# Kernel tuning notes

Hardware: AMD Instinct MI355X
Metric: run time of the kernel (lower is better)

Reference implementation:

```python
import jax, jax.numpy as jnp
import numpy as np

HIDDEN = 4096
N_HEADS = 32
N_KV_HEADS = 8
HEAD_DIM = 128
ROPE_BASE = 10000.0


def setup_inputs() -> dict:
    key = jax.random.key(0)
    k1, k2, k3, k4, k5 = jax.random.split(key, 5)
    s = 0.02  # init scale for weights
    return {
        "hidden_states": jax.random.normal(k1, (1, 2048, HIDDEN), dtype=jnp.float32),
        "Wq": jax.random.normal(k2, (N_HEADS * HEAD_DIM, HIDDEN), dtype=jnp.float32) * s,
        "Wk": jax.random.normal(k3, (N_KV_HEADS * HEAD_DIM, HIDDEN), dtype=jnp.float32) * s,
        "Wv": jax.random.normal(k4, (N_KV_HEADS * HEAD_DIM, HIDDEN), dtype=jnp.float32) * s,
        "Wo": jax.random.normal(k5, (HIDDEN, HIDDEN), dtype=jnp.float32) * s,
    }


def _rope(x, cos, sin):
    # x: [B, H, T, D]; cos/sin: [T, D/2] -> rotate split halves (Llama style)
    d2 = x.shape[-1] // 2
    x1, x2 = x[..., :d2], x[..., d2:]
    return jnp.concatenate([x1 * cos - x2 * sin, x1 * sin + x2 * cos], axis=-1)


def reference(hidden_states, Wq, Wk, Wv, Wo):
    B, T, _ = hidden_states.shape
    H, Hkv, D = N_HEADS, N_KV_HEADS, HEAD_DIM
    G = H // Hkv  # kv groups

    q = jnp.einsum("bth,qh->btq", hidden_states, Wq).reshape(B, T, H, D).transpose(0, 2, 1, 3)
    k = jnp.einsum("bth,kh->btk", hidden_states, Wk).reshape(B, T, Hkv, D).transpose(0, 2, 1, 3)
    v = jnp.einsum("bth,vh->btv", hidden_states, Wv).reshape(B, T, Hkv, D).transpose(0, 2, 1, 3)

    # RoPE (position_offset = 0)
    positions = jnp.arange(T, dtype=jnp.float32)
    inv_freq = ROPE_BASE ** (-jnp.arange(0, D, 2, dtype=jnp.float32) / D)  # [D/2]
    angles = positions[:, None] * inv_freq[None, :]                        # [T, D/2]
    cos, sin = jnp.cos(angles), jnp.sin(angles)
    q = _rope(q, cos, sin)
    k = _rope(k, cos, sin)

    # GQA attention without materializing expanded K/V: group query heads
    qg = q.reshape(B, Hkv, G, T, D)
    scale = 1.0 / jnp.sqrt(jnp.asarray(D, dtype=q.dtype))
    scores = jnp.einsum("bkgtd,bksd->bkgts", qg, k) * scale  # [B, Hkv, G, T, T]
    causal = jnp.tril(jnp.ones((T, T), dtype=bool))
    scores = jnp.where(causal, scores, jnp.finfo(scores.dtype).min)
    probs = jax.nn.softmax(scores, axis=-1)
    attn = jnp.einsum("bkgts,bksd->bkgtd", probs, v)          # [B, Hkv, G, T, D]
    attn = attn.reshape(B, H, T, D).transpose(0, 2, 1, 3).reshape(B, T, H * D)

    return jnp.einsum("btq,oq->bto", attn, Wo)
```

## Files before the change

### kernel.cpp

```cpp
#include <hip/hip_runtime.h>
#include <stdint.h>

#define T_SEQ   2048
#define HID     4096
#define NH      32
#define NKV     8
#define HD      128
#define QCOLS   6144
#define QK_SCALE 0.08838834764831845f

typedef _Float16 half_t;
typedef _Float16 half8 __attribute__((ext_vector_type(8)));
typedef _Float16 half4v __attribute__((ext_vector_type(4)));
typedef float    f32x4 __attribute__((ext_vector_type(4)));

typedef __attribute__((address_space(1))) const void cg_void;
typedef __attribute__((address_space(3))) void lds_void;

__global__ __launch_bounds__(256) void cast_all_k(const float* __restrict__ X,
                                                  const float* __restrict__ Wq,
                                                  const float* __restrict__ Wk,
                                                  const float* __restrict__ Wv,
                                                  const float* __restrict__ Wo,
                                                  half_t* __restrict__ Xh,
                                                  half_t* __restrict__ Wqkvh,
                                                  half_t* __restrict__ Woh) {
  int i = blockIdx.x * 256 + threadIdx.x;
  const float* src; half_t* dst; int off;
  if (i < 2097152)      { src = X;  dst = Xh;               off = i; }
  else if (i < 6291456) { src = Wq; dst = Wqkvh;            off = i - 2097152; }
  else if (i < 7340032) { src = Wk; dst = Wqkvh + 16777216; off = i - 6291456; }
  else if (i < 8388608) { src = Wv; dst = Wqkvh + 20971520; off = i - 7340032; }
  else                  { src = Wo; dst = Woh;              off = i - 8388608; }
  f32x4 v = *(const f32x4*)(src + (size_t)off * 4);
  half4v o;
  o[0] = (half_t)v[0]; o[1] = (half_t)v[1]; o[2] = (half_t)v[2]; o[3] = (half_t)v[3];
  *(half4v*)(dst + (size_t)off * 4) = o;
}

__global__ __launch_bounds__(256) void rope_tables_k(float* __restrict__ cs) {
  int idx = blockIdx.x * 256 + threadIdx.x;
  int t = idx >> 6, i = idx & 63;
  float inv = expf(-(float)i * 0.14391156831212787f);
  float a = (float)t * inv;
  cs[idx] = cosf(a);
  cs[131072 + idx] = sinf(a);
}

__global__ __launch_bounds__(256) void rope_vt_k(half_t* __restrict__ QKV,
                                                 const float* __restrict__ cs,
                                                 half_t* __restrict__ Vt) {
  if (blockIdx.x < 20480) {
    int idx = blockIdx.x * 256 + threadIdx.x;
    int i = idx & 63;
    int rem = idx >> 6;
    int head = rem % 40;
    int t = rem / 40;
    int colbase = (head < 32) ? head * HD : HID + (head - 32) * HD;
    size_t base = (size_t)t * QCOLS + colbase;
    float c = cs[t * 64 + i], s = cs[131072 + t * 64 + i];
    float x1 = (float)QKV[base + i];
    float x2 = (float)QKV[base + 64 + i];
    float o1 = x1 * c - x2 * s;
    float o2 = x1 * s + x2 * c;
    if (head < 32) { o1 *= QK_SCALE; o2 *= QK_SCALE; }
    QKV[base + i]      = (half_t)o1;
    QKV[base + 64 + i] = (half_t)o2;
  } else {
    int idx = (blockIdx.x - 20480) * 256 + threadIdx.x;
    int d  = idx & 127;
    int ts = (idx >> 7) & 255;
    int kh = idx >> 15;
    half8 o;
#pragma unroll
    for (int i = 0; i < 8; ++i)
      o[i] = QKV[(size_t)(ts * 8 + i) * QCOLS + HID + NKV * HD + kh * HD + d];
    *(half8*)&Vt[(size_t)kh * (HD * T_SEQ) + (size_t)d * T_SEQ + ts * 8] = o;
  }
}

template <int BM, int BN, int OUT_HALF>
__global__ __launch_bounds__(512, 2) void gemm8p_k(const half_t* __restrict__ A,
                                                   const half_t* __restrict__ Bm,
                                                   void* __restrict__ Cout,
                                                   int M, int N, int K) {
  constexpr int MF = BM / 32;
  constexpr int NF = BN / 64;
  constexpr int MH = MF / 2;
  constexpr int LA = BM / 64;
  constexpr int LB = BN / 64;
  __shared__ half_t Al[2][BM * 64];
  __shared__ half_t Bl[2][BN * 64];

  const int nbm = M / BM;
  const int nwg = nbm * (N / BN);
  const int bid = blockIdx.x;
  const int swz = (bid & 7) * (nwg >> 3) + (bid >> 3);
  const int brow = (swz % nbm) * BM;
  const int bcol = (swz / nbm) * BN;
  const int tid = threadIdx.x;
  const int lane = tid & 63, wid = tid >> 6;
  const int wr = wid >> 2, wc = wid & 3;
  const int lr = lane & 15, hi = lane >> 4;
  const int wrow = wr * (MF * 16), wcol = wc * (NF * 16);

  const half_t* Ab = A + (size_t)brow * K;
  const half_t* Bb = Bm + (size_t)bcol * K;

  f32x4 acc[MF][NF] = {};
  half8 afr[MH], bfr[NF];

#define STAGE_A(l, k0, buf) { \
    int c_ = (l) * 512 + tid; int r_ = c_ >> 3, s_ = c_ & 7; \
    __builtin_amdgcn_global_load_lds( \
      (cg_void*)(Ab + (size_t)r_ * K + (k0) + ((s_ ^ (r_ & 7)) * 8)), \
      (lds_void*)(&Al[buf][((l) * 512 + wid * 64) * 8]), 16, 0, 0); }
#define STAGE_B(l, k0, buf) { \
    int c_ = (l) * 512 + tid; int r_ = c_ >> 3, s_ = c_ & 7; \
    __builtin_amdgcn_global_load_lds( \
      (cg_void*)(Bb + (size_t)r_ * K + (k0) + ((s_ ^ (r_ & 7)) * 8)), \
      (lds_void*)(&Bl[buf][((l) * 512 + wid * 64) * 8]), 16, 0, 0); }
#define RD_A(i, mh, kk, buf) { \
    int row_ = wrow + ((mh) * MH + (i)) * 16 + lr; int ks_ = (kk) * 4 + hi; \
    afr[i] = *(const half8*)&Al[buf][row_ * 64 + ((ks_ ^ (row_ & 7)) * 8)]; }
#define RD_B(n, kk, buf) { \
    int row_ = wcol + (n) * 16 + lr; int ks_ = (kk) * 4 + hi; \
    bfr[n] = *(const half8*)&Bl[buf][row_ * 64 + ((ks_ ^ (row_ & 7)) * 8)]; }
#define MFMA_PH(mh) { \
    __builtin_amdgcn_s_setprio(1); \
    _Pragma("unroll") for (int i_ = 0; i_ < MH; ++i_) \
      _Pragma("unroll") for (int n_ = 0; n_ < NF; ++n_) \
        acc[(mh) * MH + i_][n_] = __builtin_amdgcn_mfma_f32_16x16x32_f16( \
            afr[i_], bfr[n_], acc[(mh) * MH + i_][n_], 0, 0, 0); \
    __builtin_amdgcn_s_setprio(0); }

#define DO_TILE(T, BUF) { \
    const int kn_ = ((T) + 1) * 64; const bool pf_ = ((T) + 1) < NT; \
    if (pf_) { _Pragma("unroll") for (int l_ = 0; l_ < LA; ++l_) STAGE_A(l_, kn_, (BUF) ^ 1); } \
    _Pragma("unroll") for (int n_ = 0; n_ < NF; ++n_) RD_B(n_, 0, BUF); \
    _Pragma("unroll") for (int i_ = 0; i_ < MH; ++i_) RD_A(i_, 0, 0, BUF); \
    MFMA_PH(0); \
    __builtin_amdgcn_s_barrier(); __builtin_amdgcn_sched_barrier(0); \
    if (pf_) { _Pragma("unroll") for (int l_ = 0; l_ < LB; ++l_) STAGE_B(l_, kn_, (BUF) ^ 1); } \
    _Pragma("unroll") for (int i_ = 0; i_ < MH; ++i_) RD_A(i_, 1, 0, BUF); \
    MFMA_PH(1); \
    __builtin_amdgcn_s_barrier(); __builtin_amdgcn_sched_barrier(0); \
    _Pragma("unroll") for (int n_ = 0; n_ < NF; ++n_) RD_B(n_, 1, BUF); \
    _Pragma("unroll") for (int i_ = 0; i_ < MH; ++i_) RD_A(i_, 1, 1, BUF); \
    MFMA_PH(1); \
    __builtin_amdgcn_s_barrier(); __builtin_amdgcn_sched_barrier(0); \
    _Pragma("unroll") for (int i_ = 0; i_ < MH; ++i_) RD_A(i_, 0, 1, BUF); \
    MFMA_PH(0); \
    asm volatile("s_waitcnt vmcnt(0)" ::: "memory"); \
    __syncthreads(); }

  const int NT = K / 64;
#pragma unroll
  for (int l_ = 0; l_ < LA; ++l_) STAGE_A(l_, 0, 0);
#pragma unroll
  for (int l_ = 0; l_ < LB; ++l_) STAGE_B(l_, 0, 0);
  asm volatile("s_waitcnt vmcnt(0)" ::: "memory");
  __syncthreads();

  for (int t = 0; t < NT; t += 2) {
    DO_TILE(t, 0);
    DO_TILE(t + 1, 1);
  }

#undef STAGE_A
#undef STAGE_B
#undef RD_A
#undef RD_B
#undef MFMA_PH
#undef DO_TILE

#pragma unroll
  for (int m = 0; m < MF; ++m)
#pragma unroll
    for (int n = 0; n < NF; ++n)
#pragma unroll
      for (int r = 0; r < 4; ++r) {
        int row = brow + wrow + m * 16 + hi * 4 + r;
        int col = bcol + wcol + n * 16 + lr;
        float v = acc[m][n][r];
        if (OUT_HALF) ((half_t*)Cout)[(size_t)row * N + col] = (half_t)v;
        else          ((float*)Cout)[(size_t)row * N + col] = v;
      }
}

__global__ __launch_bounds__(256, 2) void attn_k(const half_t* __restrict__ QKV,
                                                 const half_t* __restrict__ Vt,
                                                 half_t* __restrict__ Ob) {
  const int bid = blockIdx.x;
  const int qb = 31 - (bid >> 5);
  const int h  = bid & 31;
  const int kh = h >> 2;
  const int tid = threadIdx.x;
  const int lane = tid & 63;
  const int w = tid >> 6;
  const int lr = lane & 15, hi = lane >> 4;
  const int qrow = qb * 64 + w * 16;

  __shared__ half_t Klds[2][64 * 128];
  __shared__ half_t Vlds[2][128 * 64];
  __shared__ half_t Plds[4 * 16 * 72];

  const half_t* Qp  = QKV + h * HD;
  const half_t* Kp  = QKV + HID + kh * HD;
  const half_t* Vtp = Vt + (size_t)kh * (HD * T_SEQ);

  half8 qf[4];
#pragma unroll
  for (int kk = 0; kk < 4; ++kk)
    qf[kk] = *(const half8*)&Qp[(size_t)(qrow + lr) * QCOLS + kk * 32 + hi * 8];

  f32x4 acc[8] = {};
  float mrow[4], lrow[4];
#pragma unroll
  for (int r = 0; r < 4; ++r) { mrow[r] = -1e30f; lrow[r] = 0.0f; }

  half_t* Pw = &Plds[w * (16 * 72)];

#define STAGE_KV(kv0, buf) { \
    _Pragma("unroll") for (int c_ = 0; c_ < 4; ++c_) { \
      int chunk_ = c_ * 256 + tid; \
      int r_ = chunk_ >> 4, s_ = chunk_ & 15; \
      int cc_ = (s_ & 8) | ((s_ ^ r_) & 7); \
      __builtin_amdgcn_global_load_lds( \
          (cg_void*)(Kp + (size_t)((kv0) + r_) * QCOLS + cc_ * 8), \
          (lds_void*)(&Klds[buf][(c_ * 256 + w * 64) * 8]), 16, 0, 0); } \
    _Pragma("unroll") for (int c_ = 0; c_ < 4; ++c_) { \
      int chunk_ = c_ * 256 + tid; \
      int r_ = chunk_ >> 3, s_ = chunk_ & 7; \
      int cc_ = (s_ ^ r_) & 7; \
      __builtin_amdgcn_global_load_lds( \
          (cg_void*)(Vtp + (size_t)r_ * T_SEQ + (kv0) + cc_ * 8), \
          (lds_void*)(&Vlds[buf][(c_ * 256 + w * 64) * 8]), 16, 0, 0); } }

#define COMPUTE(T, BUF) { \
    const int kv0_ = (T) * 64; \
    f32x4 sc[4] = {}; \
    __builtin_amdgcn_s_setprio(1); \
    _Pragma("unroll") for (int jt_ = 0; jt_ < 4; ++jt_) \
      _Pragma("unroll") for (int kk_ = 0; kk_ < 4; ++kk_) { \
        int srow_ = jt_ * 16 + lr; \
        int sl_ = kk_ * 4 + hi; \
        int c_ = (sl_ & 8) | ((sl_ ^ srow_) & 7); \
        half8 kf_ = *(const half8*)&Klds[BUF][srow_ * 128 + c_ * 8]; \
        sc[jt_] = __builtin_amdgcn_mfma_f32_16x16x32_f16(qf[kk_], kf_, sc[jt_], 0, 0, 0); \
      } \
    __builtin_amdgcn_s_setprio(0); \
    if ((T) == qb) { \
      _Pragma("unroll") for (int jt_ = 0; jt_ < 4; ++jt_) \
        _Pragma("unroll") for (int r_ = 0; r_ < 4; ++r_) { \
          int ig_ = qrow + hi * 4 + r_; \
          int jg_ = kv0_ + jt_ * 16 + lr; \
          if (jg_ > ig_) sc[jt_][r_] = -1e30f; \
        } \
    } \
    float mx_[4]; \
    _Pragma("unroll") for (int r_ = 0; r_ < 4; ++r_) \
      mx_[r_] = fmaxf(fmaxf(sc[0][r_], sc[1][r_]), fmaxf(sc[2][r_], sc[3][r_])); \
    _Pragma("unroll") for (int off_ = 1; off_ < 16; off_ <<= 1) \
      _Pragma("unroll") for (int r_ = 0; r_ < 4; ++r_) \
        mx_[r_] = fmaxf(mx_[r_], __shfl_xor(mx_[r_], off_, 64)); \
    bool grow_ = false; \
    _Pragma("unroll") for (int r_ = 0; r_ < 4; ++r_) grow_ = grow_ || (mx_[r_] > mrow[r_]); \
    if (__any(grow_)) { \
      float scl_[4]; \
      _Pragma("unroll") for (int r_ = 0; r_ < 4; ++r_) { \
        float mn_ = fmaxf(mrow[r_], mx_[r_]); \
        scl_[r_] = __expf(mrow[r_] - mn_); \
        mrow[r_] = mn_; \
        float ls_ = 0.0f; \
        _Pragma("unroll") for (int jt_ = 0; jt_ < 4; ++jt_) { \
          sc[jt_][r_] = __expf(sc[jt_][r_] - mn_); ls_ += sc[jt_][r_]; } \
        lrow[r_] = lrow[r_] * scl_[r_] + ls_; \
      } \
      _Pragma("unroll") for (int g_ = 0; g_ < 8; ++g_) \
        _Pragma("unroll") for (int r_ = 0; r_ < 4; ++r_) acc[g_][r_] *= scl_[r_]; \
    } else { \
      _Pragma("unroll") for (int r_ = 0; r_ < 4; ++r_) { \
        float ls_ = 0.0f; \
        _Pragma("unroll") for (int jt_ = 0; jt_ < 4; ++jt_) { \
          sc[jt_][r_] = __expf(sc[jt_][r_] - mrow[r_]); ls_ += sc[jt_][r_]; } \
        lrow[r_] += ls_; \
      } \
    } \
    _Pragma("unroll") for (int jt_ = 0; jt_ < 4; ++jt_) \
      _Pragma("unroll") for (int r_ = 0; r_ < 4; ++r_) \
        Pw[(hi * 4 + r_) * 72 + jt_ * 16 + lr] = (half_t)sc[jt_][r_]; \
    half8 pf0_ = *(const half8*)&Pw[lr * 72 + hi * 8]; \
    half8 pf1_ = *(const half8*)&Pw[lr * 72 + 32 + hi * 8]; \
    __builtin_amdgcn_s_setprio(1); \
    _Pragma("unroll") for (int g_ = 0; g_ < 8; ++g_) { \
      int vrow_ = g_ * 16 + lr; \
      { int c0_ = (hi ^ vrow_) & 7; \
        half8 vf_ = *(const half8*)&Vlds[BUF][vrow_ * 64 + c0_ * 8]; \
        acc[g_] = __builtin_amdgcn_mfma_f32_16x16x32_f16(pf0_, vf_, acc[g_], 0, 0, 0); } \
      { int c1_ = ((4 + hi) ^ vrow_) & 7; \
        half8 vf_ = *(const half8*)&Vlds[BUF][vrow_ * 64 + c1_ * 8]; \
        acc[g_] = __builtin_amdgcn_mfma_f32_16x16x32_f16(pf1_, vf_, acc[g_], 0, 0, 0); } \
    } \
    __builtin_amdgcn_s_setprio(0); }

#define TILE_SYNC() { asm volatile("s_waitcnt vmcnt(0)" ::: "memory"); \
                      __builtin_amdgcn_s_barrier(); __builtin_amdgcn_sched_barrier(0); }

  const int nt = qb + 1;
  STAGE_KV(0, 0);
  TILE_SYNC();

  int t = 0;
  for (; t + 2 <= nt; t += 2) {
    STAGE_KV((t + 1) * 64, 1);
    COMPUTE(t, 0);
    TILE_SYNC();
    if (t + 2 < nt) { STAGE_KV((t + 2) * 64, 0); }
    COMPUTE(t + 1, 1);
    TILE_SYNC();
  }
  if (t < nt) { COMPUTE(t, 0); }

#undef STAGE_KV
#undef COMPUTE
#undef TILE_SYNC

  float linv[4];
#pragma unroll
  for (int r = 0; r < 4; ++r) {
    float l = lrow[r];
#pragma unroll
    for (int off = 1; off < 16; off <<= 1) l += __shfl_xor(l, off, 64);
    linv[r] = 1.0f / l;
  }
#pragma unroll
  for (int g = 0; g < 8; ++g)
#pragma unroll
    for (int r = 0; r < 4; ++r) {
      int row = qrow + hi * 4 + r;
      int col = h * HD + g * 16 + lr;
      Ob[(size_t)row * HID + col] = (half_t)(acc[g][r] * linv[r]);
    }
}

extern "C" void kernel_launch(void* const* d_in, const int* in_sizes, int n_in,
                              void* d_out, int out_size, void* d_ws, size_t ws_size,
                              hipStream_t stream) {
  const float* hs = (const float*)d_in[0];
  const float* Wq = (const float*)d_in[1];
  const float* Wk = (const float*)d_in[2];
  const float* Wv = (const float*)d_in[3];
  const float* Wo = (const float*)d_in[4];
  float* out = (float*)d_out;

  char* ws = (char*)d_ws;
  half_t* Xh    = (half_t*)(ws + 0);
  half_t* Vt    = (half_t*)(ws + 0);
  half_t* Wqkvh = (half_t*)(ws + 16777216);
  half_t* Woh   = (half_t*)(ws + 67108864);
  half_t* QKV   = (half_t*)(ws + 100663296);
  half_t* attnh = (half_t*)(ws + 125829120);
  float*  cs    = (float*)(ws + 142606336);
  if (ws_size < 143654912ull) return;

  cast_all_k<<<49152, 256, 0, stream>>>(hs, Wq, Wk, Wv, Wo, Xh, Wqkvh, Woh);
  rope_tables_k<<<512, 256, 0, stream>>>(cs);

  gemm8p_k<256, 192, 1><<<256, 512, 0, stream>>>(Xh, Wqkvh, (void*)QKV, 2048, 6144, 4096);
  rope_vt_k<<<21504, 256, 0, stream>>>(QKV, cs, Vt);
  attn_k<<<1024, 256, 0, stream>>>(QKV, Vt, attnh);
  gemm8p_k<128, 256, 0><<<256, 512, 0, stream>>>(attnh, Woh, (void*)out, 2048, 4096, 4096);
}
```

Before: 317.5 us.

## Fuse fp32-to-fp16 weight conversion into GEMM B-operand staging

Drops the separate cast pass over all weights. Each GEMM now reads the fp32 weights directly into registers, converts them to half, and writes them to LDS inside the pipelined main loop, while the A operand keeps its async global-to-LDS path. This removes a large cast kernel and its extra fp16 round trip through memory, at the cost of twice the B global traffic per tile inside the GEMMs, more registers, and conversion ALU work. The output-projection GEMM tile shape also changes from 128x256 to 256x128.

```diff
diff --git a/kernel.cpp b/kernel.cpp
--- a/kernel.cpp
+++ b/kernel.cpp
@@ -17,25 +17,13 @@
 typedef __attribute__((address_space(1))) const void cg_void;
 typedef __attribute__((address_space(3))) void lds_void;
 
-__global__ __launch_bounds__(256) void cast_all_k(const float* __restrict__ X,
-                                                  const float* __restrict__ Wq,
-                                                  const float* __restrict__ Wk,
-                                                  const float* __restrict__ Wv,
-                                                  const float* __restrict__ Wo,
-                                                  half_t* __restrict__ Xh,
-                                                  half_t* __restrict__ Wqkvh,
-                                                  half_t* __restrict__ Woh) {
+__global__ __launch_bounds__(256) void cast_x_k(const float* __restrict__ X,
+                                                half_t* __restrict__ Xh) {
   int i = blockIdx.x * 256 + threadIdx.x;
-  const float* src; half_t* dst; int off;
-  if (i < 2097152)      { src = X;  dst = Xh;               off = i; }
-  else if (i < 6291456) { src = Wq; dst = Wqkvh;            off = i - 2097152; }
-  else if (i < 7340032) { src = Wk; dst = Wqkvh + 16777216; off = i - 6291456; }
-  else if (i < 8388608) { src = Wv; dst = Wqkvh + 20971520; off = i - 7340032; }
-  else                  { src = Wo; dst = Woh;              off = i - 8388608; }
-  f32x4 v = *(const f32x4*)(src + (size_t)off * 4);
+  f32x4 v = *(const f32x4*)(X + (size_t)i * 4);
   half4v o;
   o[0] = (half_t)v[0]; o[1] = (half_t)v[1]; o[2] = (half_t)v[2]; o[3] = (half_t)v[3];
-  *(half4v*)(dst + (size_t)off * 4) = o;
+  *(half4v*)(Xh + (size_t)i * 4) = o;
 }
 
 __global__ __launch_bounds__(256) void rope_tables_k(float* __restrict__ cs) {
@@ -81,7 +69,9 @@
 
 template <int BM, int BN, int OUT_HALF>
 __global__ __launch_bounds__(512, 2) void gemm8p_k(const half_t* __restrict__ A,
-                                                   const half_t* __restrict__ Bm,
+                                                   const float* __restrict__ Bq,
+                                                   const float* __restrict__ Bk,
+                                                   const float* __restrict__ Bv,
                                                    void* __restrict__ Cout,
                                                    int M, int N, int K) {
   constexpr int MF = BM / 32;
@@ -105,21 +95,37 @@
   const int wrow = wr * (MF * 16), wcol = wc * (NF * 16);
 
   const half_t* Ab = A + (size_t)brow * K;
-  const half_t* Bb = Bm + (size_t)bcol * K;
+
+  const float* bp[LB];
+#pragma unroll
+  for (int l = 0; l < LB; ++l) {
+    int c = l * 512 + tid, r = c >> 3, s = c & 7;
+    int row = bcol + r;
+    const float* src = (row < 4096) ? (Bq + (size_t)row * K)
+                     : (row < 5120) ? (Bk + (size_t)(row - 4096) * K)
+                                    : (Bv + (size_t)(row - 5120) * K);
+    bp[l] = src + ((s ^ (r & 7)) * 8);
+  }
 
   f32x4 acc[MF][NF] = {};
   half8 afr[MH], bfr[NF];
+  f32x4 breg[LB][2];
 
 #define STAGE_A(l, k0, buf) { \
     int c_ = (l) * 512 + tid; int r_ = c_ >> 3, s_ = c_ & 7; \
     __builtin_amdgcn_global_load_lds( \
       (cg_void*)(Ab + (size_t)r_ * K + (k0) + ((s_ ^ (r_ & 7)) * 8)), \
       (lds_void*)(&Al[buf][((l) * 512 + wid * 64) * 8]), 16, 0, 0); }
-#define STAGE_B(l, k0, buf) { \
-    int c_ = (l) * 512 + tid; int r_ = c_ >> 3, s_ = c_ & 7; \
-    __builtin_amdgcn_global_load_lds( \
-      (cg_void*)(Bb + (size_t)r_ * K + (k0) + ((s_ ^ (r_ & 7)) * 8)), \
-      (lds_void*)(&Bl[buf][((l) * 512 + wid * 64) * 8]), 16, 0, 0); }
+#define LOAD_B_ALL(k0) { \
+    _Pragma("unroll") for (int l_ = 0; l_ < LB; ++l_) { \
+      breg[l_][0] = *(const f32x4*)(bp[l_] + (k0)); \
+      breg[l_][1] = *(const f32x4*)(bp[l_] + (k0) + 4); } }
+#define WRITE_B_ALL(buf) { \
+    _Pragma("unroll") for (int l_ = 0; l_ < LB; ++l_) { \
+      half8 h_; \
+      _Pragma("unroll") for (int e_ = 0; e_ < 4; ++e_) { \
+        h_[e_] = (half_t)breg[l_][0][e_]; h_[4 + e_] = (half_t)breg[l_][1][e_]; } \
+      *(half8*)&Bl[buf][((l_) * 512 + tid) * 8] = h_; } }
 #define RD_A(i, mh, kk, buf) { \
     int row_ = wrow + ((mh) * MH + (i)) * 16 + lr; int ks_ = (kk) * 4 + hi; \
     afr[i] = *(const half8*)&Al[buf][row_ * 64 + ((ks_ ^ (row_ & 7)) * 8)]; }
@@ -141,7 +147,7 @@
     _Pragma("unroll") for (int i_ = 0; i_ < MH; ++i_) RD_A(i_, 0, 0, BUF); \
     MFMA_PH(0); \
     __builtin_amdgcn_s_barrier(); __builtin_amdgcn_sched_barrier(0); \
-    if (pf_) { _Pragma("unroll") for (int l_ = 0; l_ < LB; ++l_) STAGE_B(l_, kn_, (BUF) ^ 1); } \
+    if (pf_) { LOAD_B_ALL(kn_); } \
     _Pragma("unroll") for (int i_ = 0; i_ < MH; ++i_) RD_A(i_, 1, 0, BUF); \
     MFMA_PH(1); \
     __builtin_amdgcn_s_barrier(); __builtin_amdgcn_sched_barrier(0); \
@@ -151,14 +157,15 @@
     __builtin_amdgcn_s_barrier(); __builtin_amdgcn_sched_barrier(0); \
     _Pragma("unroll") for (int i_ = 0; i_ < MH; ++i_) RD_A(i_, 0, 1, BUF); \
     MFMA_PH(0); \
+    if (pf_) { WRITE_B_ALL((BUF) ^ 1); } \
     asm volatile("s_waitcnt vmcnt(0)" ::: "memory"); \
     __syncthreads(); }
 
   const int NT = K / 64;
 #pragma unroll
   for (int l_ = 0; l_ < LA; ++l_) STAGE_A(l_, 0, 0);
-#pragma unroll
-  for (int l_ = 0; l_ < LB; ++l_) STAGE_B(l_, 0, 0);
+  LOAD_B_ALL(0);
+  WRITE_B_ALL(0);
   asm volatile("s_waitcnt vmcnt(0)" ::: "memory");
   __syncthreads();
 
@@ -168,7 +175,8 @@
   }
 
 #undef STAGE_A
-#undef STAGE_B
+#undef LOAD_B_ALL
+#undef WRITE_B_ALL
 #undef RD_A
 #undef RD_B
 #undef MFMA_PH
@@ -357,18 +365,16 @@
   char* ws = (char*)d_ws;
   half_t* Xh    = (half_t*)(ws + 0);
   half_t* Vt    = (half_t*)(ws + 0);
-  half_t* Wqkvh = (half_t*)(ws + 16777216);
-  half_t* Woh   = (half_t*)(ws + 67108864);
   half_t* QKV   = (half_t*)(ws + 100663296);
   half_t* attnh = (half_t*)(ws + 125829120);
   float*  cs    = (float*)(ws + 142606336);
   if (ws_size < 143654912ull) return;
 
-  cast_all_k<<<49152, 256, 0, stream>>>(hs, Wq, Wk, Wv, Wo, Xh, Wqkvh, Woh);
+  cast_x_k<<<8192, 256, 0, stream>>>(hs, Xh);
   rope_tables_k<<<512, 256, 0, stream>>>(cs);
 
-  gemm8p_k<256, 192, 1><<<256, 512, 0, stream>>>(Xh, Wqkvh, (void*)QKV, 2048, 6144, 4096);
+  gemm8p_k<256, 192, 1><<<256, 512, 0, stream>>>(Xh, Wq, Wk, Wv, (void*)QKV, 2048, 6144, 4096);
   rope_vt_k<<<21504, 256, 0, stream>>>(QKV, cs, Vt);
   attn_k<<<1024, 256, 0, stream>>>(QKV, Vt, attnh);
-  gemm8p_k<128, 256, 0><<<256, 512, 0, stream>>>(attnh, Woh, (void*)out, 2048, 4096, 4096);
-}
+  gemm8p_k<256, 128, 0><<<256, 512, 0, stream>>>(attnh, Wo, Wo, Wo, (void*)out, 2048, 4096, 4096);
+}
```

Result: no change. 312.8 us (-1.5%).
